# Kernel tuning notes

Measured on AMD Instinct MI355X. Metric: run time of the kernel, lower is better.

The kernel has to match this reference:

```python
import jax, jax.numpy as jnp
import numpy as np

B, L, H, NH = 2, 2048, 2048, 16
K = H // NH  # q/k head dim (num_slot) = 128
EPS = 1e-5
SCALE = K ** -0.5  # fla gla default scale = key_dim**-0.5


def setup_inputs() -> dict:
    key = jax.random.key(0)
    k0, k1, k2, k3, k4 = jax.random.split(key, 5)
    std = 0.02
    return {
        "hidden_states": jax.random.normal(k0, (B, L, H), dtype=jnp.float32),
        "Wq": jax.random.normal(k1, (K, H), dtype=jnp.float32) * std,
        "Wk": jax.random.normal(k2, (K, H), dtype=jnp.float32) * std,
        "Wog": jax.random.normal(k3, (H, H), dtype=jnp.float32) * std,
        "Wig": jax.random.normal(k4, (H, H), dtype=jnp.float32) * std,
        "g_weight": jnp.ones((H,), dtype=jnp.float32),
    }


def _gla(q, k, v, g):
    # q,k: [B,L,K]; v: [B,L,V]; g: [B,L,K] (log decay per key dim)
    # recurrence: S_t = exp(g_t)[:, :, None] * S_{t-1} + k_t^T v_t ; o_t = q_t @ S_t
    def step(S, xs):
        q_t, k_t, v_t, g_t = xs  # [B,K],[B,K],[B,V],[B,K]
        S = jnp.exp(g_t)[:, :, None] * S + k_t[:, :, None] * v_t[:, None, :]
        o_t = jnp.einsum('bk,bkv->bv', q_t, S)
        return S, o_t

    S0 = jnp.zeros((q.shape[0], q.shape[2], v.shape[2]), dtype=q.dtype)
    xs = (jnp.swapaxes(q, 0, 1), jnp.swapaxes(k, 0, 1),
          jnp.swapaxes(v, 0, 1), jnp.swapaxes(g, 0, 1))
    _, o = jax.lax.scan(step, S0, xs)  # o: [L,B,V]
    return jnp.swapaxes(o, 0, 1)


def reference(hidden_states, Wq, Wk, Wog, Wig, g_weight):
    x = hidden_states
    q = x @ Wq.T  # [B,L,K]
    k_sig = jax.nn.sigmoid(x @ Wk.T)  # k = sigmoid(k_proj(x))
    q = jax.nn.silu(q) * SCALE  # swish feature map on q; fold in GLA scale
    gf = jax.nn.log_sigmoid(-k_sig)  # per-key log decay gates
    o = _gla(q, k_sig, x, gf)  # [B,L,H] (single head, V = hidden)
    # output gate + fused RMSNorm-SwishGate
    go = o @ Wog.T + x @ Wig.T
    rms = o * jax.lax.rsqrt(jnp.mean(o * o, axis=-1, keepdims=True) + EPS) * g_weight
    return rms * go * jax.nn.sigmoid(go)
```

## Files before the change

kernel.cpp:

```cpp
#include <hip/hip_runtime.h>
#include <math.h>

#define B_ 2
#define L_ 2048
#define H_ 2048
#define KD_ 128
#define SCALE_ 0.08838834764831845f
#define EPS_ 1e-5f
#define K2_ 4096

typedef __bf16 bf16x8 __attribute__((ext_vector_type(8)));
typedef float f32x4 __attribute__((ext_vector_type(4)));

static __device__ __forceinline__ float sigmoidf_(float z) {
    return 1.0f / (1.0f + __expf(-z));
}

static __device__ __forceinline__ unsigned short f2bf(float f) {
    unsigned int u = __float_as_uint(f);
    unsigned int r = (u + 0x7fffu + ((u >> 16) & 1u)) >> 16;
    return (unsigned short)r;
}

static __device__ __forceinline__ float bf2f(unsigned short s) {
    return __uint_as_float(((unsigned int)s) << 16);
}

#define ASYNC_COPY16(gsrc, ldst)                                             \
    __builtin_amdgcn_global_load_lds(                                        \
        (const __attribute__((address_space(1))) unsigned int*)(gsrc),       \
        (__attribute__((address_space(3))) unsigned int*)(ldst), 16, 0, 0)

#define BAR()                                                                \
    do {                                                                     \
        asm volatile("" ::: "memory");                                       \
        __builtin_amdgcn_s_barrier();                                        \
        asm volatile("" ::: "memory");                                       \
    } while (0)

#define JOBA_BLKS 4096
#define JOBB_BLKS 256
#define JOBC_BLKS 4096

__global__ __launch_bounds__(256) void prep_all(
    const float* __restrict__ x, const float* __restrict__ Wq,
    const float* __restrict__ Wk, const float* __restrict__ Wog,
    const float* __restrict__ Wig, unsigned short* __restrict__ Abuf,
    unsigned short* __restrict__ Wqk, unsigned short* __restrict__ Bbuf,
    float* __restrict__ rrms_acc)
{
    const int blk = blockIdx.x;
    const float* src;
    unsigned short* dst;
    if (blk < JOBA_BLKS) {
        size_t i = (size_t)blk * 256 + threadIdx.x;
        size_t m = i >> 8, c8 = (i & 255) * 8;
        src = x + m * H_ + c8;
        dst = Abuf + m * K2_ + H_ + c8;
    } else if (blk < JOBA_BLKS + JOBB_BLKS) {
        size_t i = (size_t)(blk - JOBA_BLKS) * 256 + threadIdx.x;
        if (i < 4096) rrms_acc[i] = 0.f;
        const size_t half = (size_t)KD_ * H_ / 8;
        src = ((i < half) ? Wq : Wk) + ((i < half) ? i : i - half) * 8;
        dst = Wqk + i * 8;
    } else {
        size_t i = (size_t)(blk - JOBA_BLKS - JOBB_BLKS) * 256 + threadIdx.x;
        const size_t half = (size_t)H_ * H_ / 8;
        size_t j = (i < half) ? i : i - half;
        size_t n = j >> 8, c8 = (j & 255) * 8;
        src = ((i < half) ? Wog : Wig) + n * H_ + c8;
        dst = Bbuf + n * K2_ + ((i < half) ? 0 : H_) + c8;
    }
    float4 v0 = *(const float4*)src;
    float4 v1 = *(const float4*)(src + 4);
    ushort4 a, b;
    a.x = f2bf(v0.x); a.y = f2bf(v0.y); a.z = f2bf(v0.z); a.w = f2bf(v0.w);
    b.x = f2bf(v1.x); b.y = f2bf(v1.y); b.z = f2bf(v1.z); b.w = f2bf(v1.w);
    *(ushort4*)dst = a;
    *(ushort4*)(dst + 4) = b;
}

__global__ __launch_bounds__(512, 2) void qk_proj_mfma(
    const unsigned short* __restrict__ Abuf,
    const unsigned short* __restrict__ Wqk,
    float* __restrict__ partial)
{
    __shared__ alignas(16) unsigned short As[3 * 64 * 64];
    __shared__ alignas(16) unsigned short Bs[3 * 256 * 64];
    const int tid  = threadIdx.x;
    const int lane = tid & 63;
    const int w    = tid >> 6;
    const int wrow = w >> 2;
    const int wcol = w & 3;
    const int bid  = blockIdx.x;
    const int m0 = (bid >> 2) * 64;
    const int kz = (bid & 3) * 512;

    const int frow = lane & 15;
    const int fkb  = (lane >> 4) << 3;
    const int rxor = (lane & 7) << 3;

    const int srow = tid >> 3;
    const int scol = (((tid & 7) ^ (srow & 7)) << 3);
    const unsigned short* agsrc =
        Abuf + (size_t)(m0 + srow) * K2_ + H_ + kz + scol;
    const unsigned short* bgsrc = Wqk + (size_t)srow * H_ + kz + scol;
    unsigned short* As_dst = As + tid * 8;
    unsigned short* Bs_dst = Bs + tid * 8;

#define QSTAGE_A_(cb, k0)                                                    \
    ASYNC_COPY16(agsrc + (k0), As_dst + (cb) * 4096)
#define QSTAGE_B_(cb, k0, it_)                                               \
    ASYNC_COPY16(bgsrc + (size_t)((it_) * 64) * H_ + (k0),                   \
                 Bs_dst + (cb) * 16384 + (it_) * 4096)
#define QLDA_(buf, i_, ks_)                                                  \
    (*(const bf16x8*)(As + (buf) * 4096 +                                    \
                      (wrow * 32 + (i_) * 16 + frow) * 64 +                  \
                      (((ks_) * 32 + fkb) ^ rxor)))
#define QLDB_(buf, j_, ks_)                                                  \
    (*(const bf16x8*)(Bs + (buf) * 16384 +                                   \
                      (wcol * 64 + (j_) * 16 + frow) * 64 +                  \
                      (((ks_) * 32 + fkb) ^ rxor)))
#define MFMA_(a_, b_, c_)                                                    \
    (c_) = __builtin_amdgcn_mfma_f32_16x16x32_bf16((a_), (b_), (c_), 0, 0, 0)

    f32x4 acc[2][4] = {};

    QSTAGE_A_(0, 0);
    QSTAGE_B_(0, 0, 0); QSTAGE_B_(0, 0, 1); QSTAGE_B_(0, 0, 2); QSTAGE_B_(0, 0, 3);
    QSTAGE_A_(1, 64);
    QSTAGE_B_(1, 64, 0); QSTAGE_B_(1, 64, 1); QSTAGE_B_(1, 64, 2); QSTAGE_B_(1, 64, 3);
    asm volatile("s_waitcnt vmcnt(5)" ::: "memory");
    BAR();

    int cur = 0;
    for (int t = 0; t < 8; ++t) {
        int stg = cur + 2; if (stg >= 3) stg -= 3;
        const int kpre = (t + 2) * 64;
        const bool pre = (t + 2 < 8);
        bf16x8 af0[2], bf0[4], af1[2], bf1[4];

        #pragma unroll
        for (int i = 0; i < 2; ++i) af0[i] = QLDA_(cur, i, 0);
        #pragma unroll
        for (int j = 0; j < 4; ++j) bf0[j] = QLDB_(cur, j, 0);
        #pragma unroll
        for (int i = 0; i < 2; ++i) af1[i] = QLDA_(cur, i, 1);
        #pragma unroll
        for (int j = 0; j < 4; ++j) bf1[j] = QLDB_(cur, j, 1);

        if (pre) {
            QSTAGE_A_(stg, kpre);
            QSTAGE_B_(stg, kpre, 0);
            QSTAGE_B_(stg, kpre, 1);
            QSTAGE_B_(stg, kpre, 2);
            QSTAGE_B_(stg, kpre, 3);
        }

        __builtin_amdgcn_s_setprio(1);
        #pragma unroll
        for (int i = 0; i < 2; ++i)
            #pragma unroll
            for (int j = 0; j < 4; ++j)
                MFMA_(af0[i], bf0[j], acc[i][j]);
        #pragma unroll
        for (int i = 0; i < 2; ++i)
            #pragma unroll
            for (int j = 0; j < 4; ++j)
                MFMA_(af1[i], bf1[j], acc[i][j]);
        __builtin_amdgcn_s_setprio(0);

        if (pre) { asm volatile("s_waitcnt vmcnt(5)" ::: "memory"); }
        else     { asm volatile("s_waitcnt vmcnt(0)" ::: "memory"); }
        BAR();

        cur = cur + 1; if (cur == 3) cur = 0;
    }

#undef QSTAGE_A_
#undef QSTAGE_B_
#undef QLDA_
#undef QLDB_
#undef MFMA_

    float* pz = partial + (size_t)(bid & 3) * 4096 * 256;
    #pragma unroll
    for (int i = 0; i < 2; ++i) {
        #pragma unroll
        for (int reg = 0; reg < 4; ++reg) {
            int m = m0 + wrow * 32 + i * 16 + (lane >> 4) * 4 + reg;
            #pragma unroll
            for (int j = 0; j < 4; ++j) {
                int n = wcol * 64 + j * 16 + (lane & 15);
                pz[(size_t)m * 256 + n] = acc[i][j][reg];
            }
        }
    }
}

__global__ __launch_bounds__(256) void scan_scale_kernel(
    const float* __restrict__ partial,
    unsigned short* __restrict__ qt_b, unsigned short* __restrict__ kA_b,
    unsigned short* __restrict__ kB_b)
{
    const int c = blockIdx.x, b = blockIdx.y;
    const int kd = blockIdx.z * 32 + (threadIdx.x & 31);
    const int rg = threadIdx.x >> 5;
    const size_t stride = (size_t)4096 * 256;
    const int row0 = b * L_ + c * 64 + rg * 8;

    float qv[8], kv[8], gp[8];
    float run = 0.f;
    #pragma unroll
    for (int j = 0; j < 8; ++j) {
        size_t off = (size_t)(row0 + j) * 256;
        float sq = partial[off + kd] + partial[stride + off + kd]
                 + partial[2 * stride + off + kd] + partial[3 * stride + off + kd];
        float sk = partial[off + 128 + kd] + partial[stride + off + 128 + kd]
                 + partial[2 * stride + off + 128 + kd]
                 + partial[3 * stride + off + 128 + kd];
        float ksv = sigmoidf_(sk);
        qv[j] = sq * sigmoidf_(sq) * SCALE_;
        kv[j] = ksv;
        run += -log1pf(__expf(ksv));
        gp[j] = run;
    }
    __shared__ float s_seg[8][32];
    s_seg[rg][threadIdx.x & 31] = run;
    __syncthreads();
    float base = 0.f, total = 0.f;
    #pragma unroll
    for (int r = 0; r < 8; ++r) {
        float v = s_seg[r][threadIdx.x & 31];
        base += (r < rg) ? v : 0.f;
        total += v;
    }
    #pragma unroll
    for (int j = 0; j < 8; ++j) {
        float s = base + gp[j];
        size_t idx = (size_t)(row0 + j) * KD_ + kd;
        qt_b[idx] = f2bf(qv[j] * __expf(s));
        kA_b[idx] = f2bf(kv[j] * __expf(-s));
        kB_b[idx] = f2bf(kv[j] * __expf(total - s));
    }
}

__global__ __launch_bounds__(256) void p_kernel(
    const unsigned short* __restrict__ qt_b,
    const unsigned short* __restrict__ kA_b,
    const unsigned short* __restrict__ kB_b,
    unsigned short* __restrict__ Pbuf)
{
    const int c = blockIdx.x, b = blockIdx.y;
    const int tid = threadIdx.x;
    const int w = tid >> 6, l = tid & 63;
    const int lr = l & 15, lq = l >> 4;
    const int q0 = c * 64;
    const size_t rowbase = (size_t)b * L_;

    bf16x8 aq[4];
    {
        const unsigned short* qrow = qt_b + (rowbase + q0 + 16 * w + lr) * KD_;
        #pragma unroll
        for (int kt = 0; kt < 4; ++kt)
            aq[kt] = *(const bf16x8*)(qrow + kt * 32 + lq * 8);
    }
    unsigned short* pout = Pbuf + (size_t)(b * 32 + c) * 64 * 128;
    #pragma unroll
    for (int jt = 0; jt < 8; ++jt) {
        f32x4 p = {};
        const int si = jt * 16 + lr;
        const bool prev = (jt < 4);
        const bool dead = (c == 0 && prev);
        if (!dead) {
            int kp = prev ? (q0 - 64 + si) : (q0 + si - 64);
            const unsigned short* kb = (prev ? kB_b : kA_b) + (rowbase + kp) * KD_;
            #pragma unroll
            for (int kt = 0; kt < 4; ++kt) {
                bf16x8 bk = *(const bf16x8*)(kb + kt * 32 + lq * 8);
                p = __builtin_amdgcn_mfma_f32_16x16x32_bf16(aq[kt], bk, p, 0, 0, 0);
            }
        }
        #pragma unroll
        for (int reg = 0; reg < 4; ++reg) {
            int ti = 16 * w + lq * 4 + reg;
            bool keep = !dead && (si <= ti + 64);
            pout[ti * 128 + si] = keep ? f2bf(p[reg]) : (unsigned short)0;
        }
    }
}

#define SV_ 130

__global__ __launch_bounds__(256) void pv_kernel(
    const unsigned short* __restrict__ Pbuf,
    unsigned short* Abuf,
    float* __restrict__ rrms_acc)
{
    const int c  = blockIdx.x;
    const int b  = blockIdx.y;
    const int vt = blockIdx.z;
    const int tid = threadIdx.x;
    const int w = tid >> 6, l = tid & 63;
    const int lr = l & 15, lq = l >> 4;
    const int q0 = c * 64, kpos0 = q0 - 64, v0c = vt * 128;
    const size_t rowbase = (size_t)b * L_;

    __shared__ alignas(16) unsigned short Vt[128 * SV_];

    {
        const int a = tid & 15;
        const int kr0 = tid >> 4;
        for (int kr = kr0; kr < 128; kr += 16) {
            int kp = kpos0 + kr;
            ushort4 u0 = {0, 0, 0, 0}, u1 = {0, 0, 0, 0};
            if (kp >= 0) {
                const unsigned short* src =
                    Abuf + (rowbase + kp) * K2_ + H_ + v0c + a * 8;
                u0 = *(const ushort4*)src;
                u1 = *(const ushort4*)(src + 4);
            }
            unsigned short vals[8] = {u0.x, u0.y, u0.z, u0.w,
                                      u1.x, u1.y, u1.z, u1.w};
            #pragma unroll
            for (int j = 0; j < 8; ++j)
                Vt[(a * 8 + j) * SV_ + kr] = vals[j];
        }
    }

    bf16x8 ap[4];
    {
        const unsigned short* prow =
            Pbuf + ((size_t)(b * 32 + c) * 64 + 16 * w + lr) * 128;
        #pragma unroll
        for (int kt = 0; kt < 4; ++kt)
            ap[kt] = *(const bf16x8*)(prow + kt * 32 + lq * 8);
    }
    __syncthreads();

    float rsum[4] = {0.f, 0.f, 0.f, 0.f};
    #pragma unroll
    for (int jt = 0; jt < 8; ++jt) {
        f32x4 oa = {};
        const int n = jt * 16 + lr;
        #pragma unroll
        for (int kt = 0; kt < 4; ++kt) {
            const unsigned int* vp =
                (const unsigned int*)(Vt + n * SV_ + kt * 32 + lq * 8);
            union { unsigned int u[4]; bf16x8 v; } bb;
            bb.u[0] = vp[0]; bb.u[1] = vp[1]; bb.u[2] = vp[2]; bb.u[3] = vp[3];
            oa = __builtin_amdgcn_mfma_f32_16x16x32_bf16(ap[kt], bb.v, oa, 0, 0, 0);
        }
        #pragma unroll
        for (int reg = 0; reg < 4; ++reg) {
            int qrow = 16 * w + lq * 4 + reg;
            size_t orow = rowbase + q0 + qrow;
            float val = oa[reg];
            Abuf[orow * K2_ + v0c + n] = f2bf(val);
            rsum[reg] += val * val;
        }
    }
    #pragma unroll
    for (int mk = 1; mk < 16; mk <<= 1) {
        #pragma unroll
        for (int reg = 0; reg < 4; ++reg)
            rsum[reg] += __shfl_xor(rsum[reg], mk, 64);
    }
    if (lr == 0) {
        #pragma unroll
        for (int reg = 0; reg < 4; ++reg)
            atomicAdd(&rrms_acc[rowbase + q0 + 16 * w + lq * 4 + reg], rsum[reg]);
    }
}

__global__ __launch_bounds__(512, 2) void out_gemm_mfma(
    const unsigned short* __restrict__ Abuf,
    const unsigned short* __restrict__ Bbuf,
    const float* __restrict__ gw, const float* __restrict__ rrms_acc,
    float* __restrict__ out)
{
    __shared__ alignas(16) unsigned short As[3 * 128 * 64];
    __shared__ alignas(16) unsigned short Bs[3 * 256 * 64];
    const int tid  = threadIdx.x;
    const int lane = tid & 63;
    const int w    = tid >> 6;
    const int wrow = w >> 2;
    const int wcol = w & 3;
    const int bid  = blockIdx.x;
    const int m0 = (bid >> 3) * 128;
    const int n0 = (bid & 7) * 256;

    const int frow = lane & 15;
    const int fkb  = (lane >> 4) << 3;
    const int rxor = (lane & 7) << 3;

    const int srow = tid >> 3;
    const int scol = (((tid & 7) ^ (srow & 7)) << 3);
    const unsigned short* agsrc = Abuf + (size_t)(m0 + srow) * K2_ + scol;
    const unsigned short* bgsrc = Bbuf + (size_t)(n0 + srow) * K2_ + scol;
    unsigned short* As_dst = As + tid * 8;
    unsigned short* Bs_dst = Bs + tid * 8;

#define STAGE_A2_(cb, k0)                                                    \
    {                                                                        \
        ASYNC_COPY16(agsrc + (k0), As_dst + (cb) * 8192);                    \
        ASYNC_COPY16(agsrc + (size_t)64 * K2_ + (k0),                        \
                     As_dst + (cb) * 8192 + 4096);                           \
    }
#define STAGE_B1_(cb, k0, it_)                                               \
    ASYNC_COPY16(bgsrc + (size_t)((it_) * 64) * K2_ + (k0),                  \
                 Bs_dst + (cb) * 16384 + (it_) * 4096)
#define LDA_(buf, i_, ks_)                                                   \
    (*(const bf16x8*)(As + (buf) * 8192 +                                    \
                      (wrow * 64 + (i_) * 16 + frow) * 64 +                  \
                      (((ks_) * 32 + fkb) ^ rxor)))
#define LDB_(buf, j_, ks_)                                                   \
    (*(const bf16x8*)(Bs + (buf) * 16384 +                                   \
                      (wcol * 64 + (j_) * 16 + frow) * 64 +                  \
                      (((ks_) * 32 + fkb) ^ rxor)))
#define MFMA_(a_, b_, c_)                                                    \
    (c_) = __builtin_amdgcn_mfma_f32_16x16x32_bf16((a_), (b_), (c_), 0, 0, 0)

    f32x4 acc[4][4] = {};

    STAGE_A2_(0, 0);
    STAGE_B1_(0, 0, 0); STAGE_B1_(0, 0, 1); STAGE_B1_(0, 0, 2); STAGE_B1_(0, 0, 3);
    STAGE_A2_(1, 64);
    STAGE_B1_(1, 64, 0); STAGE_B1_(1, 64, 1); STAGE_B1_(1, 64, 2); STAGE_B1_(1, 64, 3);
    asm volatile("s_waitcnt vmcnt(6)" ::: "memory");
    BAR();

    int cur = 0;
    for (int t = 0; t < 64; ++t) {
        int stg = cur + 2; if (stg >= 3) stg -= 3;
        const int kpre = (t + 2) * 64;
        const bool pre = (t + 2 < 64);
        bf16x8 af0[4], bf0[4], af1[4], bf1[4];

        #pragma unroll
        for (int i = 0; i < 4; ++i) af0[i] = LDA_(cur, i, 0);
        #pragma unroll
        for (int j = 0; j < 4; ++j) bf0[j] = LDB_(cur, j, 0);
        #pragma unroll
        for (int i = 0; i < 4; ++i) af1[i] = LDA_(cur, i, 1);
        #pragma unroll
        for (int j = 0; j < 4; ++j) bf1[j] = LDB_(cur, j, 1);

        if (pre) {
            STAGE_A2_(stg, kpre);
            STAGE_B1_(stg, kpre, 0);
            STAGE_B1_(stg, kpre, 1);
            STAGE_B1_(stg, kpre, 2);
            STAGE_B1_(stg, kpre, 3);
        }

        __builtin_amdgcn_s_setprio(1);
        #pragma unroll
        for (int i = 0; i < 4; ++i)
            #pragma unroll
            for (int j = 0; j < 4; ++j)
                MFMA_(af0[i], bf0[j], acc[i][j]);
        #pragma unroll
        for (int i = 0; i < 4; ++i)
            #pragma unroll
            for (int j = 0; j < 4; ++j)
                MFMA_(af1[i], bf1[j], acc[i][j]);
        __builtin_amdgcn_s_setprio(0);

        if (pre) { asm volatile("s_waitcnt vmcnt(6)" ::: "memory"); }
        else     { asm volatile("s_waitcnt vmcnt(0)" ::: "memory"); }
        BAR();

        cur = cur + 1; if (cur == 3) cur = 0;
    }

#undef STAGE_A2_
#undef STAGE_B1_
#undef LDA_
#undef LDB_
#undef MFMA_

    #pragma unroll
    for (int i = 0; i < 4; ++i) {
        #pragma unroll
        for (int reg = 0; reg < 4; ++reg) {
            int m = m0 + wrow * 64 + i * 16 + (lane >> 4) * 4 + reg;
            float rv = rsqrtf(rrms_acc[m] * (1.0f / H_) + EPS_);
            #pragma unroll
            for (int j = 0; j < 4; ++j) {
                int n = n0 + wcol * 64 + j * 16 + (lane & 15);
                float go = acc[i][j][reg];
                float ov = bf2f(Abuf[(size_t)m * K2_ + n]);
                out[(size_t)m * H_ + n] = ov * rv * gw[n] * go * sigmoidf_(go);
            }
        }
    }
}

extern "C" void kernel_launch(void* const* d_in, const int* in_sizes, int n_in,
                              void* d_out, int out_size, void* d_ws, size_t ws_size,
                              hipStream_t stream) {
    (void)in_sizes; (void)n_in; (void)out_size; (void)ws_size;
    const float* x   = (const float*)d_in[0];
    const float* Wq  = (const float*)d_in[1];
    const float* Wk  = (const float*)d_in[2];
    const float* Wog = (const float*)d_in[3];
    const float* Wig = (const float*)d_in[4];
    const float* gw  = (const float*)d_in[5];
    float* out = (float*)d_out;

    const size_t MK = (size_t)B_ * L_ * KD_;
    unsigned short* Abuf = (unsigned short*)d_ws;
    unsigned short* Bbuf = Abuf + (size_t)4096 * K2_;
    unsigned short* qt_b = Bbuf + (size_t)2048 * K2_;
    unsigned short* kA_b = qt_b + MK;
    unsigned short* kB_b = kA_b + MK;
    unsigned short* Wqk  = kB_b + MK;
    unsigned short* Pbuf = Wqk + (size_t)256 * H_;
    float* partial  = (float*)(Pbuf + (size_t)64 * 64 * 128);
    float* rrms_acc = partial + (size_t)4 * 4096 * 256;

    prep_all<<<JOBA_BLKS + JOBB_BLKS + JOBC_BLKS, 256, 0, stream>>>(
        x, Wq, Wk, Wog, Wig, Abuf, Wqk, Bbuf, rrms_acc);
    qk_proj_mfma<<<256, 512, 0, stream>>>(Abuf, Wqk, partial);
    scan_scale_kernel<<<dim3(32, B_, 4), 256, 0, stream>>>(partial, qt_b, kA_b, kB_b);
    p_kernel<<<dim3(32, B_), 256, 0, stream>>>(qt_b, kA_b, kB_b, Pbuf);
    pv_kernel<<<dim3(32, B_, 16), 256, 0, stream>>>(Pbuf, Abuf, rrms_acc);
    out_gemm_mfma<<<256, 512, 0, stream>>>(Abuf, Bbuf, gw, rrms_acc, out);
}
```

Measured before the change: 231.2 us.

## Fuse P score computation into PV kernel via shared-memory P tile

Removes the separate p_kernel launch and the global Pbuf round trip by computing the chunk's P tile in each PV block and keeping it in LDS. Each block now processes two V column tiles (grid z halves from 16 to 8) so the recomputed P is amortized over two tiles. The cost is that P is recomputed 8 times per chunk instead of once, plus extra LDS use and an added barrier between V tiles.

```diff
diff --git a/kernel.cpp b/kernel.cpp
--- a/kernel.cpp
+++ b/kernel.cpp
@@ -245,121 +245,120 @@
     }
 }
 
-__global__ __launch_bounds__(256) void p_kernel(
+#define SV_ 130
+#define SP_ 136
+
+__global__ __launch_bounds__(256) void pv_fused(
     const unsigned short* __restrict__ qt_b,
     const unsigned short* __restrict__ kA_b,
     const unsigned short* __restrict__ kB_b,
-    unsigned short* __restrict__ Pbuf)
-{
-    const int c = blockIdx.x, b = blockIdx.y;
-    const int tid = threadIdx.x;
-    const int w = tid >> 6, l = tid & 63;
-    const int lr = l & 15, lq = l >> 4;
-    const int q0 = c * 64;
-    const size_t rowbase = (size_t)b * L_;
-
-    bf16x8 aq[4];
-    {
-        const unsigned short* qrow = qt_b + (rowbase + q0 + 16 * w + lr) * KD_;
-        #pragma unroll
-        for (int kt = 0; kt < 4; ++kt)
-            aq[kt] = *(const bf16x8*)(qrow + kt * 32 + lq * 8);
-    }
-    unsigned short* pout = Pbuf + (size_t)(b * 32 + c) * 64 * 128;
-    #pragma unroll
-    for (int jt = 0; jt < 8; ++jt) {
-        f32x4 p = {};
-        const int si = jt * 16 + lr;
-        const bool prev = (jt < 4);
-        const bool dead = (c == 0 && prev);
-        if (!dead) {
-            int kp = prev ? (q0 - 64 + si) : (q0 + si - 64);
-            const unsigned short* kb = (prev ? kB_b : kA_b) + (rowbase + kp) * KD_;
-            #pragma unroll
-            for (int kt = 0; kt < 4; ++kt) {
-                bf16x8 bk = *(const bf16x8*)(kb + kt * 32 + lq * 8);
-                p = __builtin_amdgcn_mfma_f32_16x16x32_bf16(aq[kt], bk, p, 0, 0, 0);
-            }
-        }
-        #pragma unroll
-        for (int reg = 0; reg < 4; ++reg) {
-            int ti = 16 * w + lq * 4 + reg;
-            bool keep = !dead && (si <= ti + 64);
-            pout[ti * 128 + si] = keep ? f2bf(p[reg]) : (unsigned short)0;
-        }
-    }
-}
-
-#define SV_ 130
-
-__global__ __launch_bounds__(256) void pv_kernel(
-    const unsigned short* __restrict__ Pbuf,
     unsigned short* Abuf,
     float* __restrict__ rrms_acc)
 {
     const int c  = blockIdx.x;
     const int b  = blockIdx.y;
-    const int vt = blockIdx.z;
+    const int vg = blockIdx.z;
     const int tid = threadIdx.x;
     const int w = tid >> 6, l = tid & 63;
     const int lr = l & 15, lq = l >> 4;
-    const int q0 = c * 64, kpos0 = q0 - 64, v0c = vt * 128;
+    const int q0 = c * 64, kpos0 = q0 - 64;
     const size_t rowbase = (size_t)b * L_;
 
+    __shared__ alignas(16) unsigned short Pl[64 * SP_];
     __shared__ alignas(16) unsigned short Vt[128 * SV_];
 
     {
-        const int a = tid & 15;
-        const int kr0 = tid >> 4;
-        for (int kr = kr0; kr < 128; kr += 16) {
-            int kp = kpos0 + kr;
-            ushort4 u0 = {0, 0, 0, 0}, u1 = {0, 0, 0, 0};
-            if (kp >= 0) {
-                const unsigned short* src =
-                    Abuf + (rowbase + kp) * K2_ + H_ + v0c + a * 8;
-                u0 = *(const ushort4*)src;
-                u1 = *(const ushort4*)(src + 4);
-            }
-            unsigned short vals[8] = {u0.x, u0.y, u0.z, u0.w,
-                                      u1.x, u1.y, u1.z, u1.w};
-            #pragma unroll
-            for (int j = 0; j < 8; ++j)
-                Vt[(a * 8 + j) * SV_ + kr] = vals[j];
-        }
-    }
+        bf16x8 aq[4];
+        const unsigned short* qrow = qt_b + (rowbase + q0 + 16 * w + lr) * KD_;
+        #pragma unroll
+        for (int kt = 0; kt < 4; ++kt)
+            aq[kt] = *(const bf16x8*)(qrow + kt * 32 + lq * 8);
+        #pragma unroll
+        for (int jt = 0; jt < 8; ++jt) {
+            f32x4 p = {};
+            const int si = jt * 16 + lr;
+            const bool prev = (jt < 4);
+            const bool dead = (c == 0 && prev);
+            if (!dead) {
+                int kp = prev ? (q0 - 64 + si) : (q0 + si - 64);
+                const unsigned short* kb =
+                    (prev ? kB_b : kA_b) + (rowbase + kp) * KD_;
+                #pragma unroll
+                for (int kt = 0; kt < 4; ++kt) {
+                    bf16x8 bk = *(const bf16x8*)(kb + kt * 32 + lq * 8);
+                    p = __builtin_amdgcn_mfma_f32_16x16x32_bf16(aq[kt], bk, p,
+                                                                0, 0, 0);
+                }
+            }
+            #pragma unroll
+            for (int reg = 0; reg < 4; ++reg) {
+                int ti = 16 * w + lq * 4 + reg;
+                bool keep = !dead && (si <= ti + 64);
+                Pl[ti * SP_ + si] = keep ? f2bf(p[reg]) : (unsigned short)0;
+            }
+        }
+    }
+    __syncthreads();
 
     bf16x8 ap[4];
-    {
-        const unsigned short* prow =
-            Pbuf + ((size_t)(b * 32 + c) * 64 + 16 * w + lr) * 128;
-        #pragma unroll
-        for (int kt = 0; kt < 4; ++kt)
-            ap[kt] = *(const bf16x8*)(prow + kt * 32 + lq * 8);
-    }
-    __syncthreads();
+    #pragma unroll
+    for (int kt = 0; kt < 4; ++kt)
+        ap[kt] = *(const bf16x8*)(Pl + (16 * w + lr) * SP_ + kt * 32 + lq * 8);
 
     float rsum[4] = {0.f, 0.f, 0.f, 0.f};
-    #pragma unroll
-    for (int jt = 0; jt < 8; ++jt) {
-        f32x4 oa = {};
-        const int n = jt * 16 + lr;
-        #pragma unroll
-        for (int kt = 0; kt < 4; ++kt) {
-            const unsigned int* vp =
-                (const unsigned int*)(Vt + n * SV_ + kt * 32 + lq * 8);
-            union { unsigned int u[4]; bf16x8 v; } bb;
-            bb.u[0] = vp[0]; bb.u[1] = vp[1]; bb.u[2] = vp[2]; bb.u[3] = vp[3];
-            oa = __builtin_amdgcn_mfma_f32_16x16x32_bf16(ap[kt], bb.v, oa, 0, 0, 0);
-        }
-        #pragma unroll
-        for (int reg = 0; reg < 4; ++reg) {
-            int qrow = 16 * w + lq * 4 + reg;
-            size_t orow = rowbase + q0 + qrow;
-            float val = oa[reg];
-            Abuf[orow * K2_ + v0c + n] = f2bf(val);
-            rsum[reg] += val * val;
-        }
-    }
+
+    #pragma unroll
+    for (int h = 0; h < 2; ++h) {
+        const int vt = vg * 2 + h;
+        const int v0c = vt * 128;
+        if (h) __syncthreads();
+
+        {
+            const int a = tid & 15;
+            const int kr0 = tid >> 4;
+            for (int kr = kr0; kr < 128; kr += 16) {
+                int kp = kpos0 + kr;
+                ushort4 u0 = {0, 0, 0, 0}, u1 = {0, 0, 0, 0};
+                if (kp >= 0) {
+                    const unsigned short* src =
+                        Abuf + (rowbase + kp) * K2_ + H_ + v0c + a * 8;
+                    u0 = *(const ushort4*)src;
+                    u1 = *(const ushort4*)(src + 4);
+                }
+                unsigned short vals[8] = {u0.x, u0.y, u0.z, u0.w,
+                                          u1.x, u1.y, u1.z, u1.w};
+                #pragma unroll
+                for (int j = 0; j < 8; ++j)
+                    Vt[(a * 8 + j) * SV_ + kr] = vals[j];
+            }
+        }
+        __syncthreads();
+
+        #pragma unroll
+        for (int jt = 0; jt < 8; ++jt) {
+            f32x4 oa = {};
+            const int n = jt * 16 + lr;
+            #pragma unroll
+            for (int kt = 0; kt < 4; ++kt) {
+                const unsigned int* vp =
+                    (const unsigned int*)(Vt + n * SV_ + kt * 32 + lq * 8);
+                union { unsigned int u[4]; bf16x8 v; } bb;
+                bb.u[0] = vp[0]; bb.u[1] = vp[1];
+                bb.u[2] = vp[2]; bb.u[3] = vp[3];
+                oa = __builtin_amdgcn_mfma_f32_16x16x32_bf16(ap[kt], bb.v, oa,
+                                                             0, 0, 0);
+            }
+            #pragma unroll
+            for (int reg = 0; reg < 4; ++reg) {
+                int qrow = 16 * w + lq * 4 + reg;
+                size_t orow = rowbase + q0 + qrow;
+                float val = oa[reg];
+                Abuf[orow * K2_ + v0c + n] = f2bf(val);
+                rsum[reg] += val * val;
+            }
+        }
+    }
+
     #pragma unroll
     for (int mk = 1; mk < 16; mk <<= 1) {
         #pragma unroll
@@ -524,7 +523,6 @@
         x, Wq, Wk, Wog, Wig, Abuf, Wqk, Bbuf, rrms_acc);
     qk_proj_mfma<<<256, 512, 0, stream>>>(Abuf, Wqk, partial);
     scan_scale_kernel<<<dim3(32, B_, 4), 256, 0, stream>>>(partial, qt_b, kA_b, kB_b);
-    p_kernel<<<dim3(32, B_), 256, 0, stream>>>(qt_b, kA_b, kB_b, Pbuf);
-    pv_kernel<<<dim3(32, B_, 16), 256, 0, stream>>>(Pbuf, Abuf, rrms_acc);
+    pv_fused<<<dim3(32, B_, 8), 256, 0, stream>>>(qt_b, kA_b, kB_b, Abuf, rrms_acc);
     out_gemm_mfma<<<256, 512, 0, stream>>>(Abuf, Bbuf, gw, rrms_acc, out);
 }
```

Result: no change. 232.1 us (+0.4%).
